# Kernel optimization log

Measured on AMD Instinct MI355X. Metric: run time of the kernel, lower is better.

The kernel has to match this reference:

```python
import jax, jax.numpy as jnp
import numpy as np

NUM_SRC = 100000
NUM_DST = 100000
NUM_EDGES = 800000
WIDTH = 128
LEAKY_SLOPE = 0.01  # torch LeakyReLU default


def setup_inputs() -> dict:
    key = jax.random.key(0)
    k1, k2, k3, k4 = jax.random.split(key, 4)
    x_src = jax.random.normal(k1, (NUM_SRC, WIDTH), dtype=jnp.float32)
    x_dst = jax.random.normal(k2, (NUM_DST, WIDTH), dtype=jnp.float32)
    e = jax.random.randint(k3, (2, NUM_EDGES), 0, NUM_DST, dtype=jnp.int64)
    W = jax.random.normal(k4, (2 * WIDTH, WIDTH), dtype=jnp.float32) * 0.02
    b = jnp.zeros((WIDTH,), dtype=jnp.float32)
    return {"x_src": x_src, "x_dst": x_dst, "e": e, "W": W, "b": b}


def reference(x_src, x_dst, e, W, b):
    src_idx, dst_idx = e[0], e[1]
    # gather + per-edge diff: [E, W]
    diffs = x_dst[dst_idx] - x_src[src_idx]
    # segment max over destination nodes; empty segments -> 0 (matches torch.zeros_like init)
    seg_max = jax.ops.segment_max(diffs, dst_idx, num_segments=NUM_DST)
    counts = jax.ops.segment_sum(jnp.ones((diffs.shape[0],), dtype=x_dst.dtype),
                                 dst_idx, num_segments=NUM_DST)
    maxes = jnp.where(counts[:, None] > 0, seg_max, jnp.zeros_like(seg_max))
    # MLP: Linear(2W -> W) + LeakyReLU, then residual
    h = jnp.concatenate([x_dst, maxes], axis=1) @ W + b
    h = jax.nn.leaky_relu(h, negative_slope=LEAKY_SLOPE)
    return x_dst + h
```

## Files before the change

### kernel.cpp

```cpp
#include <hip/hip_runtime.h>

#define WIDTH 128
#define SLOPE 0.01f
#define SBS 512
#define FBM 16
#define ECAP 512

typedef __attribute__((ext_vector_type(8))) short short8;
typedef __attribute__((ext_vector_type(4))) float f32x4;

__device__ __forceinline__ unsigned short f2bf(float f) {
    unsigned b = __float_as_uint(f);
    b += 0x7FFFu + ((b >> 16) & 1u);
    return (unsigned short)(b >> 16);
}
__device__ __forceinline__ float4 upk(uint2 u) {
    float4 r;
    r.x = __uint_as_float(u.x << 16);
    r.y = __uint_as_float(u.x & 0xFFFF0000u);
    r.z = __uint_as_float(u.y << 16);
    r.w = __uint_as_float(u.y & 0xFFFF0000u);
    return r;
}
__device__ __forceinline__ void fmin8u(float mn[8], uint4 v) {
    mn[0] = fminf(mn[0], __uint_as_float(v.x << 16));
    mn[1] = fminf(mn[1], __uint_as_float(v.x & 0xFFFF0000u));
    mn[2] = fminf(mn[2], __uint_as_float(v.y << 16));
    mn[3] = fminf(mn[3], __uint_as_float(v.y & 0xFFFF0000u));
    mn[4] = fminf(mn[4], __uint_as_float(v.z << 16));
    mn[5] = fminf(mn[5], __uint_as_float(v.z & 0xFFFF0000u));
    mn[6] = fminf(mn[6], __uint_as_float(v.w << 16));
    mn[7] = fminf(mn[7], __uint_as_float(v.w & 0xFFFF0000u));
}
__device__ __forceinline__ int swz(int lr, int bc) {
    return lr * 512 + (bc ^ ((lr & 7) << 4));
}

__global__ void prep_kernel(const float* __restrict__ x_src,
                            const float* __restrict__ W,
                            const int* __restrict__ e,
                            unsigned short* __restrict__ xsb,
                            unsigned short* __restrict__ Wt,
                            unsigned* __restrict__ counts,
                            int* __restrict__ rank,
                            int NS, int E, int nconv, int nhist) {
    int b = blockIdx.x;
    if (b < nconv) {
        int i = b * 256 + threadIdx.x;
        if (i < NS * 32) {
            float4 v = reinterpret_cast<const float4*>(x_src)[i];
            ushort4 o;
            o.x = f2bf(v.x); o.y = f2bf(v.y); o.z = f2bf(v.z); o.w = f2bf(v.w);
            *reinterpret_cast<ushort4*>(xsb + (size_t)i * 4) = o;
        }
    } else if (b < nconv + nhist) {
        int i = (b - nconv) * 256 + threadIdx.x;
        if (i < E) {
            int dst = e[E + i];
            rank[i] = (int)atomicAdd(&counts[dst], 1u);
        }
    } else {
        int t = (b - nconv - nhist) * 256 + threadIdx.x;
        if (t < 128 * 64) {
            int n = t & 127, kc = t >> 7;
            ushort4 o;
            unsigned short* op = &o.x;
            #pragma unroll
            for (int j = 0; j < 4; ++j) {
                int k = kc * 4 + j;
                float v;
                if (k < 128) v = W[(size_t)k * 128 + n] + W[(size_t)(k + 128) * 128 + n];
                else         v = -W[(size_t)k * 128 + n];
                op[j] = f2bf(v);
            }
            *reinterpret_cast<ushort4*>(Wt + (size_t)n * 256 + kc * 4) = o;
        }
    }
}

__global__ void block_sum_kernel(const unsigned* __restrict__ counts,
                                 unsigned* __restrict__ bsums, int M) {
    int i = blockIdx.x * SBS + threadIdx.x;
    unsigned v = (i < M) ? counts[i] : 0u;
    for (int d = 32; d > 0; d >>= 1) v += __shfl_down(v, d);
    __shared__ unsigned ws[SBS / 64];
    int lane = threadIdx.x & 63, w = threadIdx.x >> 6;
    if (lane == 0) ws[w] = v;
    __syncthreads();
    if (threadIdx.x == 0) {
        unsigned s = 0;
        for (int k = 0; k < SBS / 64; ++k) s += ws[k];
        bsums[blockIdx.x] = s;
    }
}

__global__ void bsum_scan_kernel(const unsigned* __restrict__ bsums,
                                 unsigned* __restrict__ bbase, int NB,
                                 int* __restrict__ offsets, int M) {
    __shared__ unsigned s[256];
    int t = threadIdx.x;
    unsigned v = (t < NB) ? bsums[t] : 0u;
    s[t] = v;
    __syncthreads();
    for (int off = 1; off < 256; off <<= 1) {
        unsigned n = (t >= off) ? s[t - off] : 0u;
        __syncthreads();
        s[t] += n;
        __syncthreads();
    }
    if (t < NB) bbase[t] = s[t] - v;
    if (t == 255) offsets[M] = (int)s[255];
}

__global__ void scan_final_kernel(const unsigned* __restrict__ counts,
                                  const unsigned* __restrict__ bbase,
                                  int* __restrict__ offsets, int M) {
    int b = blockIdx.x, t = threadIdx.x;
    int i = b * SBS + t;
    unsigned c = (i < M) ? counts[i] : 0u;
    unsigned v = c;
    int lane = t & 63, w = t >> 6;
    for (int d = 1; d < 64; d <<= 1) {
        unsigned n = __shfl_up(v, d);
        if (lane >= d) v += n;
    }
    __shared__ unsigned ws[SBS / 64];
    if (lane == 63) ws[w] = v;
    __syncthreads();
    unsigned wbase = 0;
    for (int k = 0; k < w; ++k) wbase += ws[k];
    if (i < M) offsets[i] = (int)(bbase[b] + wbase + v - c);
}

__global__ void scatter_kernel(const int* __restrict__ e,
                               const int* __restrict__ offsets,
                               const int* __restrict__ rank,
                               int* __restrict__ csr, int E) {
    int i = blockIdx.x * blockDim.x + threadIdx.x;
    if (i < E) {
        int dst = e[E + i];
        csr[offsets[dst] + rank[i]] = e[i];
    }
}

template<int XSB>
__global__ __launch_bounds__(256, 4) void fused_kernel(
        const float* __restrict__ x_src,
        const unsigned short* __restrict__ xsb,
        const float* __restrict__ x_dst,
        const int* __restrict__ offsets,
        const int* __restrict__ csr,
        const unsigned short* __restrict__ Wt,
        const float* __restrict__ bias,
        float* __restrict__ out, int M) {
    __shared__ __align__(16) unsigned short At[FBM * 256];
    __shared__ __align__(16) int eidx[ECAP];
    __shared__ int offs[FBM + 1];
    char* Ab = reinterpret_cast<char*>(At);
    int tid = threadIdx.x;
    int lane = tid & 63;
    int wv = tid >> 6;
    int blockRow = blockIdx.x * FBM;

    int ebeg = offsets[blockRow];
    int eend = offsets[blockRow + FBM];
    int ecount = eend - ebeg;
    if (tid <= FBM) offs[tid] = offsets[blockRow + tid];
    #pragma unroll
    for (int i = 0; i < FBM * 32 / 256; ++i) {
        int u = tid + 256 * i;
        int lr = u >> 5, c4 = u & 31;
        float4 v = reinterpret_cast<const float4*>(x_dst)[(size_t)(blockRow + lr) * 32 + c4];
        ushort4 o;
        o.x = f2bf(v.x); o.y = f2bf(v.y); o.z = f2bf(v.z); o.w = f2bf(v.w);
        *reinterpret_cast<ushort4*>(Ab + swz(lr, c4 * 8)) = o;
    }
    bool fit = (ecount <= ECAP);
    for (int i = tid; i < min(ecount, ECAP); i += 256) eidx[i] = csr[ebeg + i];
    __syncthreads();

    int l15 = lane & 15;
    int rg = lane >> 4;
    int lr = wv * 4 + rg;
    int rb = offs[lr] - ebeg;
    int re = offs[lr + 1] - ebeg;
    int deg = re - rb;
    int lim = re - 1;
    int oA = offs[wv * 4], oB = offs[wv * 4 + 1], oC = offs[wv * 4 + 2];
    int oD = offs[wv * 4 + 3], oE = offs[wv * 4 + 4];
    int mb = max(max(oB - oA, oC - oB), max(oD - oC, oE - oD));
    int nb4 = ((mb + 3) >> 2) << 2;

    float mn[8];
    #pragma unroll
    for (int j = 0; j < 8; ++j) mn[j] = INFINITY;

#define GLOOP(IDX)                                                          \
    for (int e0 = 0; e0 < nb4; e0 += 4) {                                   \
        int p0 = max(min(rb + e0 + 0, lim), 0);                             \
        int p1 = max(min(rb + e0 + 1, lim), 0);                             \
        int p2 = max(min(rb + e0 + 2, lim), 0);                             \
        int p3 = max(min(rb + e0 + 3, lim), 0);                             \
        int i0 = IDX(p0); int i1 = IDX(p1); int i2 = IDX(p2); int i3 = IDX(p3); \
        if (XSB) {                                                          \
            const uint4* xs = reinterpret_cast<const uint4*>(xsb);          \
            uint4 v0 = xs[(size_t)i0 * 16 + l15];                           \
            uint4 v1 = xs[(size_t)i1 * 16 + l15];                           \
            uint4 v2 = xs[(size_t)i2 * 16 + l15];                           \
            uint4 v3 = xs[(size_t)i3 * 16 + l15];                           \
            fmin8u(mn, v0); fmin8u(mn, v1); fmin8u(mn, v2); fmin8u(mn, v3); \
        } else {                                                            \
            const float4* xf = reinterpret_cast<const float4*>(x_src);      \
            float4 a0 = xf[(size_t)i0 * 32 + l15 * 2];                      \
            float4 b0 = xf[(size_t)i0 * 32 + l15 * 2 + 1];                  \
            float4 a1 = xf[(size_t)i1 * 32 + l15 * 2];                      \
            float4 b1 = xf[(size_t)i1 * 32 + l15 * 2 + 1];                  \
            float4 a2 = xf[(size_t)i2 * 32 + l15 * 2];                      \
            float4 b2 = xf[(size_t)i2 * 32 + l15 * 2 + 1];                  \
            float4 a3 = xf[(size_t)i3 * 32 + l15 * 2];                      \
            float4 b3 = xf[(size_t)i3 * 32 + l15 * 2 + 1];                  \
            a0.x = fminf(a0.x, a1.x); a0.y = fminf(a0.y, a1.y);             \
            a0.z = fminf(a0.z, a1.z); a0.w = fminf(a0.w, a1.w);             \
            a2.x = fminf(a2.x, a3.x); a2.y = fminf(a2.y, a3.y);             \
            a2.z = fminf(a2.z, a3.z); a2.w = fminf(a2.w, a3.w);             \
            mn[0] = fminf(mn[0], fminf(a0.x, a2.x));                        \
            mn[1] = fminf(mn[1], fminf(a0.y, a2.y));                        \
            mn[2] = fminf(mn[2], fminf(a0.z, a2.z));                        \
            mn[3] = fminf(mn[3], fminf(a0.w, a2.w));                        \
            b0.x = fminf(b0.x, b1.x); b0.y = fminf(b0.y, b1.y);             \
            b0.z = fminf(b0.z, b1.z); b0.w = fminf(b0.w, b1.w);             \
            b2.x = fminf(b2.x, b3.x); b2.y = fminf(b2.y, b3.y);             \
            b2.z = fminf(b2.z, b3.z); b2.w = fminf(b2.w, b3.w);             \
            mn[4] = fminf(mn[4], fminf(b0.x, b2.x));                        \
            mn[5] = fminf(mn[5], fminf(b0.y, b2.y));                        \
            mn[6] = fminf(mn[6], fminf(b0.z, b2.z));                        \
            mn[7] = fminf(mn[7], fminf(b0.w, b2.w));                        \
        }                                                                   \
    }

#define IDX_LDS(p) eidx[p]
#define IDX_GLB(p) csr[ebeg + (p)]
    if (fit) { GLOOP(IDX_LDS) } else { GLOOP(IDX_GLB) }
#undef IDX_LDS
#undef IDX_GLB
#undef GLOOP

    {
        ushort4 oa, ob;
        if (deg > 0) {
            oa.x = f2bf(mn[0]); oa.y = f2bf(mn[1]);
            oa.z = f2bf(mn[2]); oa.w = f2bf(mn[3]);
            ob.x = f2bf(mn[4]); ob.y = f2bf(mn[5]);
            ob.z = f2bf(mn[6]); ob.w = f2bf(mn[7]);
        } else {
            oa = *reinterpret_cast<const ushort4*>(Ab + swz(lr, l15 * 16));
            ob = *reinterpret_cast<const ushort4*>(Ab + swz(lr, l15 * 16 + 8));
        }
        *reinterpret_cast<ushort4*>(Ab + swz(lr, 256 + l15 * 16)) = oa;
        *reinterpret_cast<ushort4*>(Ab + swz(lr, 256 + l15 * 16 + 8)) = ob;
    }
    __syncthreads();

    int q = lane >> 4;
    int ncol0 = wv * 32;
    f32x4 acc0 = (f32x4){0.f, 0.f, 0.f, 0.f};
    f32x4 acc1 = (f32x4){0.f, 0.f, 0.f, 0.f};
    size_t b0off = (size_t)(ncol0 + l15) * 256;
    size_t b1off = (size_t)(ncol0 + 16 + l15) * 256;

    #pragma unroll
    for (int s = 0; s < 8; ++s) {
        int koff = s * 32 + q * 8;
        short8 b0 = *reinterpret_cast<const short8*>(Wt + b0off + koff);
        short8 b1 = *reinterpret_cast<const short8*>(Wt + b1off + koff);
        short8 a = *reinterpret_cast<const short8*>(Ab + swz(l15, koff * 2));
        acc0 = __builtin_amdgcn_mfma_f32_16x16x32_bf16(b0, a, acc0, 0, 0, 0);
        acc1 = __builtin_amdgcn_mfma_f32_16x16x32_bf16(b1, a, acc1, 0, 0, 0);
    }

    float4 bi0 = *reinterpret_cast<const float4*>(bias + ncol0 + q * 4);
    float4 bi1 = *reinterpret_cast<const float4*>(bias + ncol0 + 16 + q * 4);
    int row = blockRow + l15;
    #pragma unroll
    for (int u = 0; u < 2; ++u) {
        int col = ncol0 + u * 16 + q * 4;
        f32x4 av = u ? acc1 : acc0;
        float4 bv = u ? bi1 : bi0;
        uint2 xu = *reinterpret_cast<const uint2*>(Ab + swz(l15, col * 2));
        float4 xb = upk(xu);
        float4 o;
        float h;
        h = av[0] + bv.x; o.x = xb.x + (h > 0.f ? h : SLOPE * h);
        h = av[1] + bv.y; o.y = xb.y + (h > 0.f ? h : SLOPE * h);
        h = av[2] + bv.z; o.z = xb.z + (h > 0.f ? h : SLOPE * h);
        h = av[3] + bv.w; o.w = xb.w + (h > 0.f ? h : SLOPE * h);
        *reinterpret_cast<float4*>(out + (size_t)row * 128 + col) = o;
    }
}

extern "C" void kernel_launch(void* const* d_in, const int* in_sizes, int n_in,
                              void* d_out, int out_size, void* d_ws, size_t ws_size,
                              hipStream_t stream) {
    const float* x_src = (const float*)d_in[0];
    const float* x_dst = (const float*)d_in[1];
    const int*   e     = (const int*)d_in[2];
    const float* W     = (const float*)d_in[3];
    const float* bias  = (const float*)d_in[4];
    float* out = (float*)d_out;

    int NS = in_sizes[0] / WIDTH;
    int E  = in_sizes[2] / 2;
    int M  = in_sizes[1] / WIDTH;
    int NB = (M + SBS - 1) / SBS;

    unsigned short* xsb = (unsigned short*)d_ws;
    unsigned short* Wt  = xsb + (size_t)NS * WIDTH;
    unsigned* counts  = (unsigned*)(Wt + 128 * 256);
    int*      offsets = (int*)(counts + M);
    int*      rank    = offsets + (M + 1);
    int*      csr     = rank + E;
    unsigned* bsums   = (unsigned*)(csr + E);
    unsigned* bbase   = bsums + NB;
    size_t need = (char*)(bbase + NB) - (char*)d_ws;
    int use_xsb = (ws_size >= need) ? 1 : 0;
    if (!use_xsb) {
        Wt = (unsigned short*)d_ws;
        counts  = (unsigned*)(Wt + 128 * 256);
        offsets = (int*)(counts + M);
        rank    = offsets + (M + 1);
        csr     = rank + E;
        bsums   = (unsigned*)(csr + E);
        bbase   = bsums + NB;
    }

    hipMemsetAsync(counts, 0, (size_t)M * sizeof(unsigned), stream);

    int nconv = use_xsb ? (NS * 32 + 255) / 256 : 0;
    int nhist = (E + 255) / 256;
    int nwt   = (128 * 64 + 255) / 256;
    prep_kernel<<<nconv + nhist + nwt, 256, 0, stream>>>(x_src, W, e, xsb, Wt,
                                                         counts, rank, NS, E,
                                                         nconv, nhist);
    block_sum_kernel<<<NB, SBS, 0, stream>>>(counts, bsums, M);
    bsum_scan_kernel<<<1, 256, 0, stream>>>(bsums, bbase, NB, offsets, M);
    scan_final_kernel<<<NB, SBS, 0, stream>>>(counts, bbase, offsets, M);
    scatter_kernel<<<(E + 255) / 256, 256, 0, stream>>>(e, offsets, rank, csr, E);

    int fblocks = (M + FBM - 1) / FBM;
    if (use_xsb)
        fused_kernel<1><<<fblocks, 256, 0, stream>>>(x_src, xsb, x_dst, offsets,
                                                     csr, Wt, bias, out, M);
    else
        fused_kernel<0><<<fblocks, 256, 0, stream>>>(x_src, xsb, x_dst, offsets,
                                                     csr, Wt, bias, out, M);
}
```

Measured before the change: 146.7 us.

## Replace rank array with cursor atomics and widen gather loop to eight edges

Histogram no longer stores a per-edge rank. Instead the scan writes a per-node cursor and the scatter takes CSR slots with atomicAdd on that cursor, which removes E ints of write and read traffic but puts atomics into scatter and makes the order within each segment nondeterministic. The gather loop on the bf16 path now issues eight row loads per iteration into two independent min accumulators to raise memory-level parallelism. Launch bounds are raised from 4 to 6 blocks per CU, which caps registers per thread in exchange for higher occupancy.

```diff
diff --git a/kernel.cpp b/kernel.cpp
--- a/kernel.cpp
+++ b/kernel.cpp
@@ -22,15 +22,17 @@
     r.w = __uint_as_float(u.y & 0xFFFF0000u);
     return r;
 }
-__device__ __forceinline__ void fmin8u(float mn[8], uint4 v) {
-    mn[0] = fminf(mn[0], __uint_as_float(v.x << 16));
-    mn[1] = fminf(mn[1], __uint_as_float(v.x & 0xFFFF0000u));
-    mn[2] = fminf(mn[2], __uint_as_float(v.y << 16));
-    mn[3] = fminf(mn[3], __uint_as_float(v.y & 0xFFFF0000u));
-    mn[4] = fminf(mn[4], __uint_as_float(v.z << 16));
-    mn[5] = fminf(mn[5], __uint_as_float(v.z & 0xFFFF0000u));
-    mn[6] = fminf(mn[6], __uint_as_float(v.w << 16));
-    mn[7] = fminf(mn[7], __uint_as_float(v.w & 0xFFFF0000u));
+__device__ __forceinline__ float fbl(unsigned u) { return __uint_as_float(u << 16); }
+__device__ __forceinline__ float fbh(unsigned u) { return __uint_as_float(u & 0xFFFF0000u); }
+__device__ __forceinline__ void accum4(float mn[8], uint4 a, uint4 b, uint4 c, uint4 d) {
+    mn[0] = fminf(mn[0], fminf(fminf(fbl(a.x), fbl(b.x)), fminf(fbl(c.x), fbl(d.x))));
+    mn[1] = fminf(mn[1], fminf(fminf(fbh(a.x), fbh(b.x)), fminf(fbh(c.x), fbh(d.x))));
+    mn[2] = fminf(mn[2], fminf(fminf(fbl(a.y), fbl(b.y)), fminf(fbl(c.y), fbl(d.y))));
+    mn[3] = fminf(mn[3], fminf(fminf(fbh(a.y), fbh(b.y)), fminf(fbh(c.y), fbh(d.y))));
+    mn[4] = fminf(mn[4], fminf(fminf(fbl(a.z), fbl(b.z)), fminf(fbl(c.z), fbl(d.z))));
+    mn[5] = fminf(mn[5], fminf(fminf(fbh(a.z), fbh(b.z)), fminf(fbh(c.z), fbh(d.z))));
+    mn[6] = fminf(mn[6], fminf(fminf(fbl(a.w), fbl(b.w)), fminf(fbl(c.w), fbl(d.w))));
+    mn[7] = fminf(mn[7], fminf(fminf(fbh(a.w), fbh(b.w)), fminf(fbh(c.w), fbh(d.w))));
 }
 __device__ __forceinline__ int swz(int lr, int bc) {
     return lr * 512 + (bc ^ ((lr & 7) << 4));
@@ -42,7 +44,6 @@
                             unsigned short* __restrict__ xsb,
                             unsigned short* __restrict__ Wt,
                             unsigned* __restrict__ counts,
-                            int* __restrict__ rank,
                             int NS, int E, int nconv, int nhist) {
     int b = blockIdx.x;
     if (b < nconv) {
@@ -55,10 +56,7 @@
         }
     } else if (b < nconv + nhist) {
         int i = (b - nconv) * 256 + threadIdx.x;
-        if (i < E) {
-            int dst = e[E + i];
-            rank[i] = (int)atomicAdd(&counts[dst], 1u);
-        }
+        if (i < E) atomicAdd(&counts[e[E + i]], 1u);
     } else {
         int t = (b - nconv - nhist) * 256 + threadIdx.x;
         if (t < 128 * 64) {
@@ -114,7 +112,8 @@
 
 __global__ void scan_final_kernel(const unsigned* __restrict__ counts,
                                   const unsigned* __restrict__ bbase,
-                                  int* __restrict__ offsets, int M) {
+                                  int* __restrict__ offsets,
+                                  int* __restrict__ cursor, int M) {
     int b = blockIdx.x, t = threadIdx.x;
     int i = b * SBS + t;
     unsigned c = (i < M) ? counts[i] : 0u;
@@ -129,22 +128,26 @@
     __syncthreads();
     unsigned wbase = 0;
     for (int k = 0; k < w; ++k) wbase += ws[k];
-    if (i < M) offsets[i] = (int)(bbase[b] + wbase + v - c);
+    if (i < M) {
+        int o = (int)(bbase[b] + wbase + v - c);
+        offsets[i] = o;
+        cursor[i] = o;
+    }
 }
 
 __global__ void scatter_kernel(const int* __restrict__ e,
-                               const int* __restrict__ offsets,
-                               const int* __restrict__ rank,
+                               int* __restrict__ cursor,
                                int* __restrict__ csr, int E) {
     int i = blockIdx.x * blockDim.x + threadIdx.x;
     if (i < E) {
         int dst = e[E + i];
-        csr[offsets[dst] + rank[i]] = e[i];
+        int pos = atomicAdd(&cursor[dst], 1);
+        csr[pos] = e[i];
     }
 }
 
 template<int XSB>
-__global__ __launch_bounds__(256, 4) void fused_kernel(
+__global__ __launch_bounds__(256, 6) void fused_kernel(
         const float* __restrict__ x_src,
         const unsigned short* __restrict__ xsb,
         const float* __restrict__ x_dst,
@@ -189,69 +192,77 @@
     int oA = offs[wv * 4], oB = offs[wv * 4 + 1], oC = offs[wv * 4 + 2];
     int oD = offs[wv * 4 + 3], oE = offs[wv * 4 + 4];
     int mb = max(max(oB - oA, oC - oB), max(oD - oC, oE - oD));
-    int nb4 = ((mb + 3) >> 2) << 2;
-
-    float mn[8];
-    #pragma unroll
-    for (int j = 0; j < 8; ++j) mn[j] = INFINITY;
-
-#define GLOOP(IDX)                                                          \
-    for (int e0 = 0; e0 < nb4; e0 += 4) {                                   \
-        int p0 = max(min(rb + e0 + 0, lim), 0);                             \
-        int p1 = max(min(rb + e0 + 1, lim), 0);                             \
-        int p2 = max(min(rb + e0 + 2, lim), 0);                             \
-        int p3 = max(min(rb + e0 + 3, lim), 0);                             \
-        int i0 = IDX(p0); int i1 = IDX(p1); int i2 = IDX(p2); int i3 = IDX(p3); \
-        if (XSB) {                                                          \
-            const uint4* xs = reinterpret_cast<const uint4*>(xsb);          \
-            uint4 v0 = xs[(size_t)i0 * 16 + l15];                           \
-            uint4 v1 = xs[(size_t)i1 * 16 + l15];                           \
-            uint4 v2 = xs[(size_t)i2 * 16 + l15];                           \
-            uint4 v3 = xs[(size_t)i3 * 16 + l15];                           \
-            fmin8u(mn, v0); fmin8u(mn, v1); fmin8u(mn, v2); fmin8u(mn, v3); \
-        } else {                                                            \
-            const float4* xf = reinterpret_cast<const float4*>(x_src);      \
-            float4 a0 = xf[(size_t)i0 * 32 + l15 * 2];                      \
-            float4 b0 = xf[(size_t)i0 * 32 + l15 * 2 + 1];                  \
-            float4 a1 = xf[(size_t)i1 * 32 + l15 * 2];                      \
-            float4 b1 = xf[(size_t)i1 * 32 + l15 * 2 + 1];                  \
-            float4 a2 = xf[(size_t)i2 * 32 + l15 * 2];                      \
-            float4 b2 = xf[(size_t)i2 * 32 + l15 * 2 + 1];                  \
-            float4 a3 = xf[(size_t)i3 * 32 + l15 * 2];                      \
-            float4 b3 = xf[(size_t)i3 * 32 + l15 * 2 + 1];                  \
-            a0.x = fminf(a0.x, a1.x); a0.y = fminf(a0.y, a1.y);             \
-            a0.z = fminf(a0.z, a1.z); a0.w = fminf(a0.w, a1.w);             \
-            a2.x = fminf(a2.x, a3.x); a2.y = fminf(a2.y, a3.y);             \
-            a2.z = fminf(a2.z, a3.z); a2.w = fminf(a2.w, a3.w);             \
-            mn[0] = fminf(mn[0], fminf(a0.x, a2.x));                        \
-            mn[1] = fminf(mn[1], fminf(a0.y, a2.y));                        \
-            mn[2] = fminf(mn[2], fminf(a0.z, a2.z));                        \
-            mn[3] = fminf(mn[3], fminf(a0.w, a2.w));                        \
-            b0.x = fminf(b0.x, b1.x); b0.y = fminf(b0.y, b1.y);             \
-            b0.z = fminf(b0.z, b1.z); b0.w = fminf(b0.w, b1.w);             \
-            b2.x = fminf(b2.x, b3.x); b2.y = fminf(b2.y, b3.y);             \
-            b2.z = fminf(b2.z, b3.z); b2.w = fminf(b2.w, b3.w);             \
-            mn[4] = fminf(mn[4], fminf(b0.x, b2.x));                        \
-            mn[5] = fminf(mn[5], fminf(b0.y, b2.y));                        \
-            mn[6] = fminf(mn[6], fminf(b0.z, b2.z));                        \
-            mn[7] = fminf(mn[7], fminf(b0.w, b2.w));                        \
-        }                                                                   \
-    }
-
-#define IDX_LDS(p) eidx[p]
-#define IDX_GLB(p) csr[ebeg + (p)]
-    if (fit) { GLOOP(IDX_LDS) } else { GLOOP(IDX_GLB) }
-#undef IDX_LDS
-#undef IDX_GLB
-#undef GLOOP
+
+    float mnA[8], mnB[8];
+    #pragma unroll
+    for (int j = 0; j < 8; ++j) { mnA[j] = INFINITY; mnB[j] = INFINITY; }
+
+    if (XSB && fit) {
+        const uint4* xs = reinterpret_cast<const uint4*>(xsb);
+        int nb8 = ((mb + 7) >> 3) << 3;
+        for (int e0 = 0; e0 < nb8; e0 += 8) {
+            int p0 = max(min(rb + e0 + 0, lim), 0);
+            int p1 = max(min(rb + e0 + 1, lim), 0);
+            int p2 = max(min(rb + e0 + 2, lim), 0);
+            int p3 = max(min(rb + e0 + 3, lim), 0);
+            int p4 = max(min(rb + e0 + 4, lim), 0);
+            int p5 = max(min(rb + e0 + 5, lim), 0);
+            int p6 = max(min(rb + e0 + 6, lim), 0);
+            int p7 = max(min(rb + e0 + 7, lim), 0);
+            int i0 = eidx[p0]; int i1 = eidx[p1];
+            int i2 = eidx[p2]; int i3 = eidx[p3];
+            int i4 = eidx[p4]; int i5 = eidx[p5];
+            int i6 = eidx[p6]; int i7 = eidx[p7];
+            uint4 v0 = xs[(size_t)i0 * 16 + l15];
+            uint4 v1 = xs[(size_t)i1 * 16 + l15];
+            uint4 v2 = xs[(size_t)i2 * 16 + l15];
+            uint4 v3 = xs[(size_t)i3 * 16 + l15];
+            uint4 v4 = xs[(size_t)i4 * 16 + l15];
+            uint4 v5 = xs[(size_t)i5 * 16 + l15];
+            uint4 v6 = xs[(size_t)i6 * 16 + l15];
+            uint4 v7 = xs[(size_t)i7 * 16 + l15];
+            accum4(mnA, v0, v1, v2, v3);
+            accum4(mnB, v4, v5, v6, v7);
+        }
+    } else {
+        int nb2 = ((mb + 1) >> 1) << 1;
+        for (int e0 = 0; e0 < nb2; e0 += 2) {
+            int p0 = max(min(rb + e0 + 0, lim), 0);
+            int p1 = max(min(rb + e0 + 1, lim), 0);
+            int i0 = fit ? eidx[p0] : csr[ebeg + p0];
+            int i1 = fit ? eidx[p1] : csr[ebeg + p1];
+            if (XSB) {
+                const uint4* xs = reinterpret_cast<const uint4*>(xsb);
+                uint4 v0 = xs[(size_t)i0 * 16 + l15];
+                uint4 v1 = xs[(size_t)i1 * 16 + l15];
+                accum4(mnA, v0, v0, v1, v1);
+            } else {
+                const float4* xf = reinterpret_cast<const float4*>(x_src);
+                float4 a0 = xf[(size_t)i0 * 32 + l15 * 2];
+                float4 b0 = xf[(size_t)i0 * 32 + l15 * 2 + 1];
+                float4 a1 = xf[(size_t)i1 * 32 + l15 * 2];
+                float4 b1 = xf[(size_t)i1 * 32 + l15 * 2 + 1];
+                mnA[0] = fminf(mnA[0], fminf(a0.x, a1.x));
+                mnA[1] = fminf(mnA[1], fminf(a0.y, a1.y));
+                mnA[2] = fminf(mnA[2], fminf(a0.z, a1.z));
+                mnA[3] = fminf(mnA[3], fminf(a0.w, a1.w));
+                mnA[4] = fminf(mnA[4], fminf(b0.x, b1.x));
+                mnA[5] = fminf(mnA[5], fminf(b0.y, b1.y));
+                mnA[6] = fminf(mnA[6], fminf(b0.z, b1.z));
+                mnA[7] = fminf(mnA[7], fminf(b0.w, b1.w));
+            }
+        }
+    }
+    #pragma unroll
+    for (int j = 0; j < 8; ++j) mnA[j] = fminf(mnA[j], mnB[j]);
 
     {
         ushort4 oa, ob;
         if (deg > 0) {
-            oa.x = f2bf(mn[0]); oa.y = f2bf(mn[1]);
-            oa.z = f2bf(mn[2]); oa.w = f2bf(mn[3]);
-            ob.x = f2bf(mn[4]); ob.y = f2bf(mn[5]);
-            ob.z = f2bf(mn[6]); ob.w = f2bf(mn[7]);
+            oa.x = f2bf(mnA[0]); oa.y = f2bf(mnA[1]);
+            oa.z = f2bf(mnA[2]); oa.w = f2bf(mnA[3]);
+            ob.x = f2bf(mnA[4]); ob.y = f2bf(mnA[5]);
+            ob.z = f2bf(mnA[6]); ob.w = f2bf(mnA[7]);
         } else {
             oa = *reinterpret_cast<const ushort4*>(Ab + swz(lr, l15 * 16));
             ob = *reinterpret_cast<const ushort4*>(Ab + swz(lr, l15 * 16 + 8));
@@ -317,8 +328,8 @@
     unsigned short* Wt  = xsb + (size_t)NS * WIDTH;
     unsigned* counts  = (unsigned*)(Wt + 128 * 256);
     int*      offsets = (int*)(counts + M);
-    int*      rank    = offsets + (M + 1);
-    int*      csr     = rank + E;
+    int*      cursor  = offsets + (M + 1);
+    int*      csr     = cursor + M;
     unsigned* bsums   = (unsigned*)(csr + E);
     unsigned* bbase   = bsums + NB;
     size_t need = (char*)(bbase + NB) - (char*)d_ws;
@@ -327,8 +338,8 @@
         Wt = (unsigned short*)d_ws;
         counts  = (unsigned*)(Wt + 128 * 256);
         offsets = (int*)(counts + M);
-        rank    = offsets + (M + 1);
-        csr     = rank + E;
+        cursor  = offsets + (M + 1);
+        csr     = cursor + M;
         bsums   = (unsigned*)(csr + E);
         bbase   = bsums + NB;
     }
@@ -339,12 +350,12 @@
     int nhist = (E + 255) / 256;
     int nwt   = (128 * 64 + 255) / 256;
     prep_kernel<<<nconv + nhist + nwt, 256, 0, stream>>>(x_src, W, e, xsb, Wt,
-                                                         counts, rank, NS, E,
+                                                         counts, NS, E,
                                                          nconv, nhist);
     block_sum_kernel<<<NB, SBS, 0, stream>>>(counts, bsums, M);
     bsum_scan_kernel<<<1, 256, 0, stream>>>(bsums, bbase, NB, offsets, M);
-    scan_final_kernel<<<NB, SBS, 0, stream>>>(counts, bbase, offsets, M);
-    scatter_kernel<<<(E + 255) / 256, 256, 0, stream>>>(e, offsets, rank, csr, E);
+    scan_final_kernel<<<NB, SBS, 0, stream>>>(counts, bbase, offsets, cursor, M);
+    scatter_kernel<<<(E + 255) / 256, 256, 0, stream>>>(e, cursor, csr, E);
 
     int fblocks = (M + FBM - 1) / FBM;
     if (use_xsb)
```

New measurement: 191.0 us. 30.2% more time.

## Use order-preserving bf16 mapping with packed u16 min and deeper gather batching

Applied to the files above, without the earlier changes.

Stores x_src in bf16 with a sign-flip mapping so float ordering becomes unsigned ordering. The segment-min then uses v_pk_min_u16, which handles two features per instruction. The gather loop is restructured to issue 16 independent loads up front, then batches of 8, to raise memory-level parallelism. This adds more register pressure from the 16 uint4 loads in flight, and the bit mapping has to be undone before writing the min into the MMA input tile.

```diff
diff --git a/kernel.cpp b/kernel.cpp
--- a/kernel.cpp
+++ b/kernel.cpp
@@ -22,15 +22,24 @@
     r.w = __uint_as_float(u.y & 0xFFFF0000u);
     return r;
 }
-__device__ __forceinline__ void fmin8u(float mn[8], uint4 v) {
-    mn[0] = fminf(mn[0], __uint_as_float(v.x << 16));
-    mn[1] = fminf(mn[1], __uint_as_float(v.x & 0xFFFF0000u));
-    mn[2] = fminf(mn[2], __uint_as_float(v.y << 16));
-    mn[3] = fminf(mn[3], __uint_as_float(v.y & 0xFFFF0000u));
-    mn[4] = fminf(mn[4], __uint_as_float(v.z << 16));
-    mn[5] = fminf(mn[5], __uint_as_float(v.z & 0xFFFF0000u));
-    mn[6] = fminf(mn[6], __uint_as_float(v.w << 16));
-    mn[7] = fminf(mn[7], __uint_as_float(v.w & 0xFFFF0000u));
+__device__ __forceinline__ unsigned short map16(unsigned short x) {
+    return (x & 0x8000u) ? (unsigned short)(~x) : (unsigned short)(x | 0x8000u);
+}
+__device__ __forceinline__ unsigned short unmap16(unsigned u) {
+    return (unsigned short)((u & 0x8000u) ? (u ^ 0x8000u) : (~u & 0xFFFFu));
+}
+__device__ __forceinline__ unsigned pkmin(unsigned a, unsigned b) {
+    unsigned r;
+    asm("v_pk_min_u16 %0, %1, %2" : "=v"(r) : "v"(a), "v"(b));
+    return r;
+}
+__device__ __forceinline__ uint4 pk4(uint4 a, uint4 b) {
+    uint4 r;
+    r.x = pkmin(a.x, b.x);
+    r.y = pkmin(a.y, b.y);
+    r.z = pkmin(a.z, b.z);
+    r.w = pkmin(a.w, b.w);
+    return r;
 }
 __device__ __forceinline__ int swz(int lr, int bc) {
     return lr * 512 + (bc ^ ((lr & 7) << 4));
@@ -50,7 +59,8 @@
         if (i < NS * 32) {
             float4 v = reinterpret_cast<const float4*>(x_src)[i];
             ushort4 o;
-            o.x = f2bf(v.x); o.y = f2bf(v.y); o.z = f2bf(v.z); o.w = f2bf(v.w);
+            o.x = map16(f2bf(v.x)); o.y = map16(f2bf(v.y));
+            o.z = map16(f2bf(v.z)); o.w = map16(f2bf(v.w));
             *reinterpret_cast<ushort4*>(xsb + (size_t)i * 4) = o;
         }
     } else if (b < nconv + nhist) {
@@ -189,69 +199,77 @@
     int oA = offs[wv * 4], oB = offs[wv * 4 + 1], oC = offs[wv * 4 + 2];
     int oD = offs[wv * 4 + 3], oE = offs[wv * 4 + 4];
     int mb = max(max(oB - oA, oC - oB), max(oD - oC, oE - oD));
-    int nb4 = ((mb + 3) >> 2) << 2;
-
-    float mn[8];
-    #pragma unroll
-    for (int j = 0; j < 8; ++j) mn[j] = INFINITY;
-
-#define GLOOP(IDX)                                                          \
-    for (int e0 = 0; e0 < nb4; e0 += 4) {                                   \
-        int p0 = max(min(rb + e0 + 0, lim), 0);                             \
-        int p1 = max(min(rb + e0 + 1, lim), 0);                             \
-        int p2 = max(min(rb + e0 + 2, lim), 0);                             \
-        int p3 = max(min(rb + e0 + 3, lim), 0);                             \
-        int i0 = IDX(p0); int i1 = IDX(p1); int i2 = IDX(p2); int i3 = IDX(p3); \
-        if (XSB) {                                                          \
-            const uint4* xs = reinterpret_cast<const uint4*>(xsb);          \
-            uint4 v0 = xs[(size_t)i0 * 16 + l15];                           \
-            uint4 v1 = xs[(size_t)i1 * 16 + l15];                           \
-            uint4 v2 = xs[(size_t)i2 * 16 + l15];                           \
-            uint4 v3 = xs[(size_t)i3 * 16 + l15];                           \
-            fmin8u(mn, v0); fmin8u(mn, v1); fmin8u(mn, v2); fmin8u(mn, v3); \
-        } else {                                                            \
-            const float4* xf = reinterpret_cast<const float4*>(x_src);      \
-            float4 a0 = xf[(size_t)i0 * 32 + l15 * 2];                      \
-            float4 b0 = xf[(size_t)i0 * 32 + l15 * 2 + 1];                  \
-            float4 a1 = xf[(size_t)i1 * 32 + l15 * 2];                      \
-            float4 b1 = xf[(size_t)i1 * 32 + l15 * 2 + 1];                  \
-            float4 a2 = xf[(size_t)i2 * 32 + l15 * 2];                      \
-            float4 b2 = xf[(size_t)i2 * 32 + l15 * 2 + 1];                  \
-            float4 a3 = xf[(size_t)i3 * 32 + l15 * 2];                      \
-            float4 b3 = xf[(size_t)i3 * 32 + l15 * 2 + 1];                  \
-            a0.x = fminf(a0.x, a1.x); a0.y = fminf(a0.y, a1.y);             \
-            a0.z = fminf(a0.z, a1.z); a0.w = fminf(a0.w, a1.w);             \
-            a2.x = fminf(a2.x, a3.x); a2.y = fminf(a2.y, a3.y);             \
-            a2.z = fminf(a2.z, a3.z); a2.w = fminf(a2.w, a3.w);             \
-            mn[0] = fminf(mn[0], fminf(a0.x, a2.x));                        \
-            mn[1] = fminf(mn[1], fminf(a0.y, a2.y));                        \
-            mn[2] = fminf(mn[2], fminf(a0.z, a2.z));                        \
-            mn[3] = fminf(mn[3], fminf(a0.w, a2.w));                        \
-            b0.x = fminf(b0.x, b1.x); b0.y = fminf(b0.y, b1.y);             \
-            b0.z = fminf(b0.z, b1.z); b0.w = fminf(b0.w, b1.w);             \
-            b2.x = fminf(b2.x, b3.x); b2.y = fminf(b2.y, b3.y);             \
-            b2.z = fminf(b2.z, b3.z); b2.w = fminf(b2.w, b3.w);             \
-            mn[4] = fminf(mn[4], fminf(b0.x, b2.x));                        \
-            mn[5] = fminf(mn[5], fminf(b0.y, b2.y));                        \
-            mn[6] = fminf(mn[6], fminf(b0.z, b2.z));                        \
-            mn[7] = fminf(mn[7], fminf(b0.w, b2.w));                        \
-        }                                                                   \
-    }
-
-#define IDX_LDS(p) eidx[p]
-#define IDX_GLB(p) csr[ebeg + (p)]
-    if (fit) { GLOOP(IDX_LDS) } else { GLOOP(IDX_GLB) }
-#undef IDX_LDS
-#undef IDX_GLB
-#undef GLOOP
+
+    uint4 mnv = make_uint4(~0u, ~0u, ~0u, ~0u);
+
+    if (XSB) {
+        if (mb > 0) {
+            const uint4* xs = reinterpret_cast<const uint4*>(xsb);
+            int ix[16];
+            #pragma unroll
+            for (int j = 0; j < 16; ++j) {
+                int p = max(min(rb + j, lim), 0);
+                ix[j] = fit ? eidx[p] : csr[ebeg + p];
+            }
+            uint4 v[16];
+            #pragma unroll
+            for (int j = 0; j < 16; ++j) v[j] = xs[(size_t)ix[j] * 16 + l15];
+            #pragma unroll
+            for (int s = 8; s >= 1; s >>= 1)
+                #pragma unroll
+                for (int j = 0; j < s; ++j) v[j] = pk4(v[j], v[j + s]);
+            mnv = v[0];
+            for (int e0 = 16; e0 < mb; e0 += 8) {
+                uint4 t[8];
+                #pragma unroll
+                for (int j = 0; j < 8; ++j) {
+                    int p = max(min(rb + e0 + j, lim), 0);
+                    int iv = fit ? eidx[p] : csr[ebeg + p];
+                    t[j] = xs[(size_t)iv * 16 + l15];
+                }
+                #pragma unroll
+                for (int s = 4; s >= 1; s >>= 1)
+                    #pragma unroll
+                    for (int j = 0; j < s; ++j) t[j] = pk4(t[j], t[j + s]);
+                mnv = pk4(mnv, t[0]);
+            }
+        }
+    } else {
+        float mn[8];
+        #pragma unroll
+        for (int j = 0; j < 8; ++j) mn[j] = INFINITY;
+        const float4* xf = reinterpret_cast<const float4*>(x_src);
+        for (int e0 = 0; e0 < mb; e0 += 2) {
+            int p0 = max(min(rb + e0 + 0, lim), 0);
+            int p1 = max(min(rb + e0 + 1, lim), 0);
+            int i0 = fit ? eidx[p0] : csr[ebeg + p0];
+            int i1 = fit ? eidx[p1] : csr[ebeg + p1];
+            float4 a0 = xf[(size_t)i0 * 32 + l15 * 2];
+            float4 b0 = xf[(size_t)i0 * 32 + l15 * 2 + 1];
+            float4 a1 = xf[(size_t)i1 * 32 + l15 * 2];
+            float4 b1 = xf[(size_t)i1 * 32 + l15 * 2 + 1];
+            mn[0] = fminf(mn[0], fminf(a0.x, a1.x));
+            mn[1] = fminf(mn[1], fminf(a0.y, a1.y));
+            mn[2] = fminf(mn[2], fminf(a0.z, a1.z));
+            mn[3] = fminf(mn[3], fminf(a0.w, a1.w));
+            mn[4] = fminf(mn[4], fminf(b0.x, b1.x));
+            mn[5] = fminf(mn[5], fminf(b0.y, b1.y));
+            mn[6] = fminf(mn[6], fminf(b0.z, b1.z));
+            mn[7] = fminf(mn[7], fminf(b0.w, b1.w));
+        }
+        mnv.x = (unsigned)map16(f2bf(mn[0])) | ((unsigned)map16(f2bf(mn[1])) << 16);
+        mnv.y = (unsigned)map16(f2bf(mn[2])) | ((unsigned)map16(f2bf(mn[3])) << 16);
+        mnv.z = (unsigned)map16(f2bf(mn[4])) | ((unsigned)map16(f2bf(mn[5])) << 16);
+        mnv.w = (unsigned)map16(f2bf(mn[6])) | ((unsigned)map16(f2bf(mn[7])) << 16);
+    }
 
     {
         ushort4 oa, ob;
         if (deg > 0) {
-            oa.x = f2bf(mn[0]); oa.y = f2bf(mn[1]);
-            oa.z = f2bf(mn[2]); oa.w = f2bf(mn[3]);
-            ob.x = f2bf(mn[4]); ob.y = f2bf(mn[5]);
-            ob.z = f2bf(mn[6]); ob.w = f2bf(mn[7]);
+            oa.x = unmap16(mnv.x & 0xFFFFu); oa.y = unmap16(mnv.x >> 16);
+            oa.z = unmap16(mnv.y & 0xFFFFu); oa.w = unmap16(mnv.y >> 16);
+            ob.x = unmap16(mnv.z & 0xFFFFu); ob.y = unmap16(mnv.z >> 16);
+            ob.z = unmap16(mnv.w & 0xFFFFu); ob.w = unmap16(mnv.w >> 16);
         } else {
             oa = *reinterpret_cast<const ushort4*>(Ab + swz(lr, l15 * 16));
             ob = *reinterpret_cast<const ushort4*>(Ab + swz(lr, l15 * 16 + 8));
```

After: 146.9 us. About the same (+0.2%).
